# Performance work log

Hardware: AMD Instinct MI355X
Metric: run time of the kernel (lower is better)

The kernel has to match this reference:

```python
import jax, jax.numpy as jnp
import numpy as np

OBS_DIM = 4096
NUM_ACTIONS = 18
ACTION_DIM = 64
D_MODEL = 512
N_LAYERS = 4
HIST = 256
BATCH = 32
D_STATE = 16
D_CONV = 4
EXPAND = 2
D_INNER = EXPAND * D_MODEL           # 1024
DT_RANK = -(-D_MODEL // 16)          # ceil(512/16)=32
OBS_OUT = D_MODEL - ACTION_DIM       # 448


def setup_inputs() -> dict:
    key = jax.random.key(0)
    ks = jax.random.split(key, 16)
    s = 0.02
    inp = {
        "obss": jax.random.normal(ks[0], (BATCH, HIST, OBS_DIM), jnp.float32),
        "actions": jax.random.randint(ks[1], (BATCH, HIST, 1), 0, NUM_ACTIONS),
        "obs_W": jax.random.normal(ks[2], (OBS_OUT, OBS_DIM), jnp.float32) * s,
        "obs_b": jnp.zeros((OBS_OUT,), jnp.float32),
        "act_emb": jax.random.normal(ks[3], (NUM_ACTIONS, ACTION_DIM), jnp.float32) * s,
        "pos_emb": jax.random.normal(ks[4], (1, HIST, D_MODEL), jnp.float32) * s,
        # stacked Mamba params, leading dim = N_LAYERS
        "W_in": jax.random.normal(ks[5], (N_LAYERS, 2 * D_INNER, D_MODEL), jnp.float32) * s,
        "conv_w": jax.random.normal(ks[6], (N_LAYERS, D_INNER, D_CONV), jnp.float32) * s,
        "conv_b": jnp.zeros((N_LAYERS, D_INNER), jnp.float32),
        "W_x": jax.random.normal(ks[7], (N_LAYERS, DT_RANK + 2 * D_STATE, D_INNER), jnp.float32) * s,
        "W_dt": jax.random.normal(ks[8], (N_LAYERS, D_INNER, DT_RANK), jnp.float32) * s,
        "b_dt": jnp.full((N_LAYERS, D_INNER), -4.6, jnp.float32),  # softplus(-4.6)~0.01
        "A_log": jnp.log(jnp.broadcast_to(jnp.arange(1, D_STATE + 1, dtype=jnp.float32), (N_LAYERS, D_INNER, D_STATE))),
        "D_p": jnp.ones((N_LAYERS, D_INNER), jnp.float32),
        "W_out": jax.random.normal(ks[9], (N_LAYERS, D_MODEL, D_INNER), jnp.float32) * s,
        "ffn_W1": jax.random.normal(ks[10], (D_MODEL, D_MODEL), jnp.float32) * s,
        "ffn_b1": jnp.zeros((D_MODEL,), jnp.float32),
        "ffn_W2": jax.random.normal(ks[11], (NUM_ACTIONS, D_MODEL), jnp.float32) * s,
        "ffn_b2": jnp.zeros((NUM_ACTIONS,), jnp.float32),
    }
    return inp


def mamba_block(x, W_in, conv_w, conv_b, W_x, W_dt, b_dt, A_log, D_p, W_out):
    # x: (B, L, D_MODEL)
    B_, L, _ = x.shape
    xz = jnp.einsum('bld,ed->ble', x, W_in)            # (B,L,2*Di)
    xi, z = jnp.split(xz, 2, axis=-1)
    # causal depthwise conv1d, kernel D_CONV
    xp = jnp.pad(xi, ((0, 0), (D_CONV - 1, 0), (0, 0)))
    xc = conv_b + sum(conv_w[:, k] * xp[:, k:k + L, :] for k in range(D_CONV))
    xc = jax.nn.silu(xc)                               # (B,L,Di)
    xdbl = jnp.einsum('bld,ed->ble', xc, W_x)          # (B,L,dt_rank+2*ds)
    dt, Bm, Cm = jnp.split(xdbl, [DT_RANK, DT_RANK + D_STATE], axis=-1)
    dt = jax.nn.softplus(jnp.einsum('blr,dr->bld', dt, W_dt) + b_dt)  # (B,L,Di)
    A = -jnp.exp(A_log)                                # (Di,ds)

    def step(h, inp):
        dt_t, B_t, C_t, x_t = inp                      # (B,Di),(B,ds),(B,ds),(B,Di)
        dA = jnp.exp(dt_t[:, :, None] * A)             # (B,Di,ds)
        h = dA * h + dt_t[:, :, None] * B_t[:, None, :] * x_t[:, :, None]
        y = jnp.einsum('bdn,bn->bd', h, C_t)
        return h, y

    h0 = jnp.zeros((B_, D_INNER, D_STATE), xc.dtype)
    xs = (dt.transpose(1, 0, 2), Bm.transpose(1, 0, 2),
          Cm.transpose(1, 0, 2), xc.transpose(1, 0, 2))
    _, ys = jax.lax.scan(step, h0, xs)                 # (L,B,Di)
    y = ys.transpose(1, 0, 2) + xc * D_p
    y = y * jax.nn.silu(z)
    return jnp.einsum('bld,ed->ble', y, W_out)         # (B,L,D_MODEL)


def reference(obss, actions, obs_W, obs_b, act_emb, pos_emb, W_in, conv_w, conv_b,
              W_x, W_dt, b_dt, A_log, D_p, W_out, ffn_W1, ffn_b1, ffn_W2, ffn_b2):
    L = obss.shape[1]
    tok = jnp.einsum('blo,eo->ble', obss, obs_W) + obs_b          # (B,L,448)
    ae = act_emb[actions[:, :, 0]]                                # (B,L,64)
    # torch.roll(ae, 1, 1) with first step zeroed (history_len > 1)
    ae = jnp.concatenate([jnp.zeros_like(ae[:, :1]), ae[:, :-1]], axis=1)
    x = jnp.concatenate([ae, tok], axis=-1) + pos_emb[:, :L, :]   # (B,L,512)
    for i in range(N_LAYERS):
        x = mamba_block(x, W_in[i], conv_w[i], conv_b[i], W_x[i], W_dt[i],
                        b_dt[i], A_log[i], D_p[i], W_out[i])
    h = jax.nn.relu(jnp.einsum('bld,ed->ble', x, ffn_W1) + ffn_b1)
    out = jnp.einsum('bld,ed->ble', h, ffn_W2) + ffn_b2           # (B,L,18)
    return out[:, -L:, :]
```

## Files before the change

### kernel.cpp

```cpp
#include <hip/hip_runtime.h>
#include <hip/hip_bf16.h>
#include <cstdint>
#include <cstddef>

#define HIST    256
#define DMODEL  512
#define DINNER  1024
#define DSTATE  16
#define DTRANK  32
#define OBSDIM  4096
#define OBSOUT  448
#define ADIM    64
#define NLAYERS 4
#define MROWS   8192

typedef __bf16  bf16x8 __attribute__((ext_vector_type(8)));
typedef float   f32x4  __attribute__((ext_vector_type(4)));

enum { MEPI_TOK = 0, MEPI_BF16 = 1, MEPI_SPLIT = 2, MEPI_RELUB = 3, MEPI_PART = 4 };

__device__ __forceinline__ float siluf(float x) { return x / (1.f + __expf(-x)); }
__device__ __forceinline__ float softplusf(float x) {
    return fmaxf(x, 0.f) + log1pf(__expf(-fabsf(x)));
}
__device__ __forceinline__ float bflo(unsigned u) { return __uint_as_float(u << 16); }
__device__ __forceinline__ float bfhi(unsigned u) { return __uint_as_float(u & 0xffff0000u); }

template<int EPI, int NW>
__global__ __launch_bounds__(256)
void gemm_mfma(const __hip_bfloat16* __restrict__ A, int lda,
               const __hip_bfloat16* __restrict__ W,
               float* __restrict__ Cf, int ldc,
               __hip_bfloat16* __restrict__ Cb, int ldcb,
               int coff, int N, int K, int nbn,
               const float* __restrict__ bias, const float* __restrict__ pos)
{
    constexpr int MI = (NW == 128) ? 4 : 2;
    __shared__ __hip_bfloat16 Asm[2][128 * 32];
    __shared__ __hip_bfloat16 Bsm[2][NW * 32];
    const int bid = blockIdx.x;
    const int xcd = bid & 7;
    const int s   = bid >> 3;
    int n_blk, m_blk, kc_ = 0;
    if constexpr (EPI == MEPI_PART) {
        m_blk = xcd * 8 + (s >> 2);
        kc_   = s & 3;
        n_blk = 0;
    } else {
        n_blk = s % nbn;
        m_blk = xcd * ((int)(gridDim.x >> 3) / nbn) + s / nbn;
    }
    const int m0 = m_blk * 128;
    const int n0 = n_blk * NW;

    const int tid  = threadIdx.x;
    const int lane = tid & 63;
    const int wv   = tid >> 6;
    const int wm   = (NW == 128) ? ((wv >> 1) << 6) : (wv << 5);
    const int wn   = (NW == 128) ? ((wv & 1) << 6) : 0;
    const int sr   = lane >> 2;
    const int scs  = (((lane & 3) ^ ((lane >> 4) & 3)) << 3);
    const int quad = lane >> 4;
    const int c16  = lane & 15;

    f32x4 acc[MI][4] = {};
    const __hip_bfloat16* aptr = A + (size_t)(m0 + wv * 16 + sr) * lda + scs + kc_ * 256;
    const __hip_bfloat16* bptr = W + (size_t)(n0 + wv * 16 + sr) * K + scs;

#define STAGE(K0, BUF) { \
    __hip_bfloat16* asml = Asm[BUF] + wv * 16 * 32; \
    __hip_bfloat16* bsml = Bsm[BUF] + wv * 16 * 32; \
    __builtin_amdgcn_global_load_lds( \
        (const __attribute__((address_space(1))) void*)(aptr + (K0)), \
        (__attribute__((address_space(3))) void*)(asml), 16, 0, 0); \
    __builtin_amdgcn_global_load_lds( \
        (const __attribute__((address_space(1))) void*)(aptr + (size_t)64 * lda + (K0)), \
        (__attribute__((address_space(3))) void*)(asml + 64 * 32), 16, 0, 0); \
    __builtin_amdgcn_global_load_lds( \
        (const __attribute__((address_space(1))) void*)(bptr + (K0)), \
        (__attribute__((address_space(3))) void*)(bsml), 16, 0, 0); \
    if (NW == 128) \
        __builtin_amdgcn_global_load_lds( \
            (const __attribute__((address_space(1))) void*)(bptr + (size_t)64 * K + (K0)), \
            (__attribute__((address_space(3))) void*)(bsml + 64 * 32), 16, 0, 0); \
    }

    STAGE(0, 0)
    int cur = 0;
    for (int k0 = 0; k0 < K; k0 += 32) {
        if (k0 + 32 < K) {
            STAGE(k0 + 32, cur ^ 1)
            if constexpr (NW == 128) asm volatile("s_waitcnt vmcnt(4)" ::: "memory");
            else                     asm volatile("s_waitcnt vmcnt(3)" ::: "memory");
        } else {
            asm volatile("s_waitcnt vmcnt(0)" ::: "memory");
        }
        __builtin_amdgcn_s_barrier();
        __builtin_amdgcn_sched_barrier(0);

        bf16x8 af[MI], bfr[4];
        #pragma unroll
        for (int i = 0; i < MI; ++i) {
            const int csw = ((quad ^ ((c16 >> 2) & 3)) << 3);
            af[i]  = *(const bf16x8*)(Asm[cur] + (wm + i * 16 + c16) * 32 + csw);
        }
        #pragma unroll
        for (int j = 0; j < 4; ++j) {
            const int csw = ((quad ^ ((c16 >> 2) & 3)) << 3);
            bfr[j] = *(const bf16x8*)(Bsm[cur] + (wn + j * 16 + c16) * 32 + csw);
        }
        #pragma unroll
        for (int i = 0; i < MI; ++i)
            #pragma unroll
            for (int j = 0; j < 4; ++j)
                acc[i][j] = __builtin_amdgcn_mfma_f32_16x16x32_bf16(af[i], bfr[j], acc[i][j], 0, 0, 0);

        __builtin_amdgcn_sched_barrier(0);
        __builtin_amdgcn_s_barrier();
        cur ^= 1;
    }
#undef STAGE

    #pragma unroll
    for (int i = 0; i < MI; ++i) {
        const int mbase = m0 + wm + i * 16 + quad * 4;
        #pragma unroll
        for (int j = 0; j < 4; ++j) {
            const int n = n0 + wn + j * 16 + c16;
            if (n < N) {
                #pragma unroll
                for (int r = 0; r < 4; ++r) {
                    const size_t m = mbase + r;
                    float v = acc[i][j][r];
                    if (EPI == MEPI_TOK) {
                        v += bias[n] + pos[(m & (HIST - 1)) * DMODEL + coff + n];
                        Cb[m * ldcb + coff + n] = __float2bfloat16(v);
                    } else if (EPI == MEPI_BF16) {
                        Cb[m * ldcb + n] = __float2bfloat16(v);
                    } else if (EPI == MEPI_SPLIT) {
                        if (n < DTRANK) Cf[m * 32 + n] = v;
                        else Cb[(m >> 1) * 64 + (n & 15) * 4 + (m & 1) * 2 + ((n >> 4) & 1)]
                                 = __float2bfloat16(v);
                    } else if (EPI == MEPI_PART) {
                        Cf[((size_t)kc_ * MROWS + m) * 64 + n] = v;
                    } else {
                        Cb[m * ldcb + n] = __float2bfloat16(fmaxf(v + bias[n], 0.f));
                    }
                }
            }
        }
    }
}

__global__ __launch_bounds__(256)
void combine_split_kernel(const float* __restrict__ p, float* __restrict__ xdt,
                          __hip_bfloat16* __restrict__ bcb)
{
    const int idx = blockIdx.x * 256 + threadIdx.x;
    const int m  = idx >> 4;
    const int n4 = (idx & 15) << 2;
    const float4 a = *(const float4*)(p + (size_t)m * 64 + n4);
    const float4 b = *(const float4*)(p + ((size_t)MROWS + m) * 64 + n4);
    const float4 c = *(const float4*)(p + ((size_t)2 * MROWS + m) * 64 + n4);
    const float4 d = *(const float4*)(p + ((size_t)3 * MROWS + m) * 64 + n4);
    const float v[4] = { a.x + b.x + c.x + d.x, a.y + b.y + c.y + d.y,
                         a.z + b.z + c.z + d.z, a.w + b.w + c.w + d.w };
    if (n4 < 32) {
        *(float4*)(xdt + (size_t)m * 32 + n4) = make_float4(v[0], v[1], v[2], v[3]);
    } else {
        #pragma unroll
        for (int j = 0; j < 4; ++j) {
            const int n = n4 + j;
            bcb[(m >> 1) * 64 + (n & 15) * 4 + (m & 1) * 2 + ((n >> 4) & 1)]
                = __float2bfloat16(v[j]);
        }
    }
}

__global__ __launch_bounds__(256)
void gemm_f32_sp(const float* __restrict__ A, int lda,
                 const float* __restrict__ W,
                 __hip_bfloat16* __restrict__ C, int ldc,
                 int N, int K, const float* __restrict__ bias)
{
    __shared__ float As[32][68];
    __shared__ float Ws[32][68];
    const int tid = threadIdx.x;
    const int tx = tid & 15, ty = tid >> 4;
    const int m0 = blockIdx.y * 64;
    const int n0 = blockIdx.x * 64;
    const int lr = tid >> 3;
    const int lc = (tid & 7) << 2;
    float acc[4][4] = {};
    for (int k0 = 0; k0 < K; k0 += 32) {
        const float4 a0 = *(const float4*)(A + (size_t)(m0 + lr) * lda + k0 + lc);
        const float4 a1 = *(const float4*)(A + (size_t)(m0 + lr + 32) * lda + k0 + lc);
        const float4 b0 = *(const float4*)(W + (size_t)(n0 + lr) * K + k0 + lc);
        const float4 b1 = *(const float4*)(W + (size_t)(n0 + lr + 32) * K + k0 + lc);
        __syncthreads();
        As[lc+0][lr] = a0.x; As[lc+1][lr] = a0.y; As[lc+2][lr] = a0.z; As[lc+3][lr] = a0.w;
        As[lc+0][lr+32] = a1.x; As[lc+1][lr+32] = a1.y; As[lc+2][lr+32] = a1.z; As[lc+3][lr+32] = a1.w;
        Ws[lc+0][lr] = b0.x; Ws[lc+1][lr] = b0.y; Ws[lc+2][lr] = b0.z; Ws[lc+3][lr] = b0.w;
        Ws[lc+0][lr+32] = b1.x; Ws[lc+1][lr+32] = b1.y; Ws[lc+2][lr+32] = b1.z; Ws[lc+3][lr+32] = b1.w;
        __syncthreads();
        #pragma unroll
        for (int k = 0; k < 32; ++k) {
            const float4 a4 = *(const float4*)&As[k][ty << 2];
            const float4 b4 = *(const float4*)&Ws[k][tx << 2];
            const float a[4] = {a4.x, a4.y, a4.z, a4.w};
            const float b[4] = {b4.x, b4.y, b4.z, b4.w};
            #pragma unroll
            for (int i = 0; i < 4; ++i)
                #pragma unroll
                for (int j = 0; j < 4; ++j)
                    acc[i][j] = fmaf(a[i], b[j], acc[i][j]);
        }
    }
    const int mb = m0 + (ty << 2);
    const int nb = n0 + (tx << 2);
    #pragma unroll
    for (int i = 0; i < 4; ++i) {
        const size_t m = mb + i;
        #pragma unroll
        for (int j = 0; j < 4; ++j) {
            const int n = nb + j;
            C[m * ldc + n] = __float2bfloat16(softplusf(acc[i][j] + bias[n]));
        }
    }
}

__global__ __launch_bounds__(256)
void cast_bf16_kernel(const float* __restrict__ src, __hip_bfloat16* __restrict__ dst, int n4)
{
    const int i = blockIdx.x * 256 + threadIdx.x;
    if (i >= n4) return;
    const float4 v = ((const float4*)src)[i];
    union { __hip_bfloat16 h[4]; short4 s; } o;
    o.h[0] = __float2bfloat16(v.x); o.h[1] = __float2bfloat16(v.y);
    o.h[2] = __float2bfloat16(v.z); o.h[3] = __float2bfloat16(v.w);
    ((short4*)dst)[i] = o.s;
}

__global__ __launch_bounds__(256)
void cast_pad_kernel(const float* __restrict__ src, __hip_bfloat16* __restrict__ dst,
                     int nrows, int K4, int total4)
{
    const int i = blockIdx.x * 256 + threadIdx.x;
    if (i >= total4) return;
    const int row = i / K4;
    float4 v = make_float4(0.f, 0.f, 0.f, 0.f);
    if (row < nrows) v = ((const float4*)src)[i];
    union { __hip_bfloat16 h[4]; short4 s; } o;
    o.h[0] = __float2bfloat16(v.x); o.h[1] = __float2bfloat16(v.y);
    o.h[2] = __float2bfloat16(v.z); o.h[3] = __float2bfloat16(v.w);
    ((short4*)dst)[i] = o.s;
}

__global__ __launch_bounds__(256)
void embed_kernel(const int* __restrict__ actions, const float* __restrict__ act_emb,
                  const float* __restrict__ pos_emb, __hip_bfloat16* __restrict__ xb)
{
    const int idx = blockIdx.x * 256 + threadIdx.x;
    const int e = idx & 63;
    const int m = idx >> 6;
    const int l = m & (HIST - 1);
    const int b = m >> 8;
    float v = pos_emb[l * DMODEL + e];
    if (l > 0) {
        const int a = actions[b * HIST + l - 1];
        v += act_emb[a * ADIM + e];
    }
    xb[(size_t)m * DMODEL + e] = __float2bfloat16(v);
}

__global__ __launch_bounds__(256)
void conv_silu_kernel(const __hip_bfloat16* __restrict__ xzb, const float* __restrict__ cw,
                      const float* __restrict__ cb, __hip_bfloat16* __restrict__ xcb)
{
    const int idx = blockIdx.x * 256 + threadIdx.x;
    const int d = idx & (DINNER - 1);
    const int m = idx >> 10;
    const int l = m & (HIST - 1);
    const float4 w = ((const float4*)cw)[d];
    const __hip_bfloat16* basep = xzb + (size_t)m * (2 * DINNER) + d;
    float acc = cb[d] + w.w * __bfloat162float(basep[0]);
    if (l >= 1) acc = fmaf(w.z, __bfloat162float(basep[-2 * DINNER]), acc);
    if (l >= 2) acc = fmaf(w.y, __bfloat162float(basep[-4 * DINNER]), acc);
    if (l >= 3) acc = fmaf(w.x, __bfloat162float(basep[-6 * DINNER]), acc);
    xcb[idx] = __float2bfloat16(siluf(acc));
}

#define DPPA(x, CTRL) { float _t; \
    asm("v_add_f32_dpp %0, %1, %1 " CTRL " row_mask:0xf bank_mask:0xf" \
        : "=v"(_t) : "v"(x)); x = _t; }

__global__ __launch_bounds__(256)
void scan_kernel(const __hip_bfloat16* __restrict__ dtb, const __hip_bfloat16* __restrict__ bcb,
                 const __hip_bfloat16* __restrict__ xcb, const __hip_bfloat16* __restrict__ zb,
                 const float* __restrict__ A_log, const float* __restrict__ D_p,
                 __hip_bfloat16* __restrict__ yb)
{
    __shared__ unsigned sdx[2][16][68];
    __shared__ unsigned sbc[2][16][68];

    const int tid = threadIdx.x;
    const int n   = tid & 15;
    const int g   = tid >> 4;

    const int bid = blockIdx.x;
    const int blk = ((bid & 7) << 8) | (bid >> 3);
    const int c0  = blk * 16;
    const int b   = c0 >> 10;
    const int d0  = c0 & (DINNER - 1);
    const int d   = d0 + g;
    const size_t row0 = (size_t)b * HIST;

    const int sr = tid >> 2;
    const int sq = tid & 3;
    const unsigned short* dtu = (const unsigned short*)dtb;
    const unsigned short* xcu = (const unsigned short*)xcb;
    const unsigned short* zu  = (const unsigned short*)zb;
    const unsigned*       bcu = (const unsigned*)bcb;

    const float Ar = -__expf(A_log[d * DSTATE + n]);
#if __has_builtin(__builtin_amdgcn_exp2f)
    const float A2 = Ar * 1.44269504089f;
#define DAEXP(x) __builtin_amdgcn_exp2f((x) * A2)
#else
#define DAEXP(x) __expf((x) * Ar)
#endif
    const float Dp = D_p[d];
    float h = 0.f;

    uint2 dv, xv; uint4 bv;
    unsigned short za[4], znx[4];

#define SLOAD(cc) { \
    const size_t rb = (row0 + (size_t)(cc) * 64 + sr) * DINNER + d0 + sq * 4; \
    dv = *(const uint2*)(dtu + rb); \
    xv = *(const uint2*)(xcu + rb); \
    bv = *(const uint4*)(bcu + row0 * 16 + (size_t)(cc) * 1024 + tid * 4); \
}
#define SWRITE(bb) { \
    const int ch = sq * 4; \
    sdx[bb][ch + 0][sr] = (dv.x & 0xffffu) | (xv.x << 16); \
    sdx[bb][ch + 1][sr] = (dv.x >> 16)     | (xv.x & 0xffff0000u); \
    sdx[bb][ch + 2][sr] = (dv.y & 0xffffu) | (xv.y << 16); \
    sdx[bb][ch + 3][sr] = (dv.y >> 16)     | (xv.y & 0xffff0000u); \
    const int e2 = (tid & 7) * 2, p2 = (tid >> 3) * 2; \
    sbc[bb][e2 + 0][p2 + 0] = bv.x; \
    sbc[bb][e2 + 0][p2 + 1] = bv.y; \
    sbc[bb][e2 + 1][p2 + 0] = bv.z; \
    sbc[bb][e2 + 1][p2 + 1] = bv.w; \
}
#define ZLOAD(cc, arr) { \
    _Pragma("unroll") \
    for (int w = 0; w < 4; ++w) \
        arr[w] = zu[(row0 + (size_t)(cc) * 64 + w * 16 + n) * (2 * DINNER) + d0 + g]; \
}
#define SSTEP(Q, R, KK) { \
    const float dt = bflo(Q), xc = bfhi(Q); \
    const float Bv = bflo(R), Cv = bfhi(R); \
    const float dA = DAEXP(dt); \
    h = fmaf(dA, h, dt * xc * Bv); \
    float ctr = h * Cv; \
    DPPA(ctr, "quad_perm:[1,0,3,2]") \
    DPPA(ctr, "quad_perm:[2,3,0,1]") \
    DPPA(ctr, "row_half_mirror") \
    DPPA(ctr, "row_mirror") \
    if (n == (KK)) yreg = ctr; \
}

    SLOAD(0)
    ZLOAD(0, za)
    SWRITE(0)
    __syncthreads();

    for (int c = 0; c < 4; ++c) {
        const int buf = c & 1;
        if (c < 3) { SLOAD(c + 1) ZLOAD(c + 1, znx) }

        const unsigned (*sdxc)[68] = sdx[buf];
        const unsigned (*sbcc)[68] = sbc[buf];
        #pragma unroll
        for (int w = 0; w < 4; ++w) {
            float yreg = 0.f;
            #pragma unroll
            for (int jq = 0; jq < 4; ++jq) {
                const uint4 qv = *(const uint4*)&sdxc[g][w * 16 + jq * 4];
                const uint4 rv = *(const uint4*)&sbcc[n][w * 16 + jq * 4];
                SSTEP(qv.x, rv.x, jq * 4 + 0)
                SSTEP(qv.y, rv.y, jq * 4 + 1)
                SSTEP(qv.z, rv.z, jq * 4 + 2)
                SSTEP(qv.w, rv.w, jq * 4 + 3)
            }
            const float xcf = bfhi(sdxc[g][w * 16 + n]);
            const float ze  = __uint_as_float((unsigned)za[w] << 16);
            yb[(row0 + c * 64 + w * 16 + n) * DINNER + d] =
                __float2bfloat16((yreg + xcf * Dp) * siluf(ze));
        }

        if (c < 3) SWRITE((c + 1) & 1)
        __syncthreads();
        #pragma unroll
        for (int w = 0; w < 4; ++w) za[w] = znx[w];
    }
#undef SLOAD
#undef SWRITE
#undef ZLOAD
#undef SSTEP
#undef DAEXP
}

__global__ __launch_bounds__(256)
void ffn2_kernel(const __hip_bfloat16* __restrict__ h, const float* __restrict__ W2,
                 const float* __restrict__ b2, float* __restrict__ out)
{
    const int idx = blockIdx.x * 256 + threadIdx.x;
    const int n = idx & 31;
    const int m = idx >> 5;
    if (n >= 18) return;
    const unsigned short* hr = (const unsigned short*)(h + (size_t)m * DMODEL);
    const float* wr = W2 + (size_t)n * DMODEL;
    float acc = b2[n];
    for (int k = 0; k < DMODEL; k += 8) {
        const uint4 hv = *(const uint4*)(hr + k);
        const float4 w0 = *(const float4*)(wr + k);
        const float4 w1 = *(const float4*)(wr + k + 4);
        acc = fmaf(bflo(hv.x), w0.x, acc);
        acc = fmaf(bfhi(hv.x), w0.y, acc);
        acc = fmaf(bflo(hv.y), w0.z, acc);
        acc = fmaf(bfhi(hv.y), w0.w, acc);
        acc = fmaf(bflo(hv.z), w1.x, acc);
        acc = fmaf(bfhi(hv.z), w1.y, acc);
        acc = fmaf(bflo(hv.w), w1.z, acc);
        acc = fmaf(bfhi(hv.w), w1.w, acc);
    }
    out[(size_t)m * 18 + n] = acc;
}

extern "C" void kernel_launch(void* const* d_in, const int* in_sizes, int n_in,
                              void* d_out, int out_size, void* d_ws, size_t ws_size,
                              hipStream_t stream)
{
    const float* obss    = (const float*)d_in[0];
    const int*   actions = (const int*)  d_in[1];
    const float* obs_W   = (const float*)d_in[2];
    const float* obs_b   = (const float*)d_in[3];
    const float* act_emb = (const float*)d_in[4];
    const float* pos_emb = (const float*)d_in[5];
    const float* W_in    = (const float*)d_in[6];
    const float* conv_w  = (const float*)d_in[7];
    const float* conv_b  = (const float*)d_in[8];
    const float* W_x     = (const float*)d_in[9];
    const float* W_dt    = (const float*)d_in[10];
    const float* b_dt    = (const float*)d_in[11];
    const float* A_log   = (const float*)d_in[12];
    const float* D_p     = (const float*)d_in[13];
    const float* W_out   = (const float*)d_in[14];
    const float* ffn_W1  = (const float*)d_in[15];
    const float* ffn_b1  = (const float*)d_in[16];
    const float* ffn_W2  = (const float*)d_in[17];
    const float* ffn_b2  = (const float*)d_in[18];
    float* out = (float*)d_out;

    const size_t MiB = 1024 * 1024;
    char* base = (char*)d_ws;
    __hip_bfloat16* xb    = (__hip_bfloat16*)(base);
    __hip_bfloat16* xzb   = (__hip_bfloat16*)(base + 8 * MiB);
    __hip_bfloat16* xcb   = (__hip_bfloat16*)(base + 40 * MiB);
    __hip_bfloat16* dtb   = (__hip_bfloat16*)(base + 56 * MiB);
    __hip_bfloat16* yb    = (__hip_bfloat16*)(base + 88 * MiB);
    float*          xdt   = (float*)(base + 104 * MiB);
    __hip_bfloat16* bcb   = (__hip_bfloat16*)(base + 105 * MiB);
    __hip_bfloat16* wbuf  = (__hip_bfloat16*)(base + 106 * MiB);
    __hip_bfloat16* wxb   = (__hip_bfloat16*)(base + 110 * MiB);
    float*          xdtp  = (float*)(base + 112 * MiB);
    __hip_bfloat16* obssb = (__hip_bfloat16*)(base + 8 * MiB);
    __hip_bfloat16* hbuf  = (__hip_bfloat16*)(base + 8 * MiB);

    cast_bf16_kernel<<<(MROWS * OBSDIM / 4) / 256, 256, 0, stream>>>(obss, obssb, MROWS * OBSDIM / 4);
    cast_pad_kernel<<<(512 * OBSDIM / 4) / 256, 256, 0, stream>>>(obs_W, wbuf, OBSOUT, OBSDIM / 4, 512 * OBSDIM / 4);
    embed_kernel<<<MROWS * ADIM / 256, 256, 0, stream>>>(actions, act_emb, pos_emb, xb);
    gemm_mfma<MEPI_TOK, 64><<<8 * (MROWS / 128), 256, 0, stream>>>(
        obssb, OBSDIM, wbuf, nullptr, 0, xb, DMODEL, ADIM, OBSOUT, OBSDIM, 8, obs_b, pos_emb);

    for (int i = 0; i < NLAYERS; ++i) {
        cast_bf16_kernel<<<(2 * DINNER * DMODEL / 4) / 256, 256, 0, stream>>>(
            W_in + (size_t)i * 2 * DINNER * DMODEL, wbuf, 2 * DINNER * DMODEL / 4);
        gemm_mfma<MEPI_BF16, 128><<<(2 * DINNER / 128) * (MROWS / 128), 256, 0, stream>>>(
            xb, DMODEL, wbuf, nullptr, 0, xzb, 2 * DINNER, 0, 2 * DINNER, DMODEL,
            2 * DINNER / 128, nullptr, nullptr);
        conv_silu_kernel<<<MROWS * DINNER / 256, 256, 0, stream>>>(
            xzb, conv_w + (size_t)i * DINNER * 4, conv_b + (size_t)i * DINNER, xcb);
        cast_pad_kernel<<<(128 * DINNER / 4) / 256, 256, 0, stream>>>(
            W_x + (size_t)i * 64 * DINNER, wxb, 64, DINNER / 4, 128 * DINNER / 4);
        gemm_mfma<MEPI_PART, 64><<<256, 256, 0, stream>>>(
            xcb, DINNER, wxb, xdtp, 0, nullptr, 0, 0, 64, 256, 1, nullptr, nullptr);
        combine_split_kernel<<<MROWS * 16 / 256, 256, 0, stream>>>(xdtp, xdt, bcb);
        gemm_f32_sp<<<dim3(DINNER / 64, MROWS / 64), 256, 0, stream>>>(
            xdt, 32, W_dt + (size_t)i * DINNER * DTRANK, dtb, DINNER, DINNER, DTRANK,
            b_dt + (size_t)i * DINNER);
        scan_kernel<<<(32 * DINNER) / 16, 256, 0, stream>>>(
            dtb, bcb, xcb, xzb + DINNER, A_log + (size_t)i * DINNER * DSTATE,
            D_p + (size_t)i * DINNER, yb);
        cast_bf16_kernel<<<(DMODEL * DINNER / 4) / 256, 256, 0, stream>>>(
            W_out + (size_t)i * DMODEL * DINNER, wbuf, DMODEL * DINNER / 4);
        gemm_mfma<MEPI_BF16, 64><<<(DMODEL / 64) * (MROWS / 128), 256, 0, stream>>>(
            yb, DINNER, wbuf, nullptr, 0, xb, DMODEL, 0, DMODEL, DINNER,
            DMODEL / 64, nullptr, nullptr);
    }

    cast_bf16_kernel<<<(DMODEL * DMODEL / 4) / 256, 256, 0, stream>>>(ffn_W1, wbuf, DMODEL * DMODEL / 4);
    gemm_mfma<MEPI_RELUB, 64><<<(DMODEL / 64) * (MROWS / 128), 256, 0, stream>>>(
        xb, DMODEL, wbuf, nullptr, 0, hbuf, DMODEL, 0, DMODEL, DMODEL,
        DMODEL / 64, ffn_b1, nullptr);
    ffn2_kernel<<<MROWS * 32 / 256, 256, 0, stream>>>(hbuf, ffn_W2, ffn_b2, out);
}
```

Baseline: 1.143 ms.

## Deepen GEMM global-to-LDS pipeline from double to quad buffering

The MFMA GEMM used to stage one K-tile ahead with two LDS buffers. It now keeps three tiles in flight across four LDS buffers, with vmcnt waits adjusted to match, and drains the last tiles in an explicit epilogue. The aim is to hide more global-memory latency behind MFMA work. In exchange, LDS use per block doubles, which may cut occupancy, and the epilogue assumes K is at least 96.

```diff
diff --git a/kernel.cpp b/kernel.cpp
--- a/kernel.cpp
+++ b/kernel.cpp
@@ -36,8 +36,8 @@
                const float* __restrict__ bias, const float* __restrict__ pos)
 {
     constexpr int MI = (NW == 128) ? 4 : 2;
-    __shared__ __hip_bfloat16 Asm[2][128 * 32];
-    __shared__ __hip_bfloat16 Bsm[2][NW * 32];
+    __shared__ __hip_bfloat16 Asm[4][128 * 32];
+    __shared__ __hip_bfloat16 Bsm[4][NW * 32];
     const int bid = blockIdx.x;
     const int xcd = bid & 7;
     const int s   = bid >> 3;
@@ -85,40 +85,43 @@
             (__attribute__((address_space(3))) void*)(bsml + 64 * 32), 16, 0, 0); \
     }
 
-    STAGE(0, 0)
-    int cur = 0;
-    for (int k0 = 0; k0 < K; k0 += 32) {
-        if (k0 + 32 < K) {
-            STAGE(k0 + 32, cur ^ 1)
-            if constexpr (NW == 128) asm volatile("s_waitcnt vmcnt(4)" ::: "memory");
-            else                     asm volatile("s_waitcnt vmcnt(3)" ::: "memory");
-        } else {
-            asm volatile("s_waitcnt vmcnt(0)" ::: "memory");
-        }
+    auto kstep = [&](int buf) {
         __builtin_amdgcn_s_barrier();
         __builtin_amdgcn_sched_barrier(0);
-
         bf16x8 af[MI], bfr[4];
-        #pragma unroll
-        for (int i = 0; i < MI; ++i) {
-            const int csw = ((quad ^ ((c16 >> 2) & 3)) << 3);
-            af[i]  = *(const bf16x8*)(Asm[cur] + (wm + i * 16 + c16) * 32 + csw);
-        }
-        #pragma unroll
-        for (int j = 0; j < 4; ++j) {
-            const int csw = ((quad ^ ((c16 >> 2) & 3)) << 3);
-            bfr[j] = *(const bf16x8*)(Bsm[cur] + (wn + j * 16 + c16) * 32 + csw);
-        }
+        const int csw = ((quad ^ ((c16 >> 2) & 3)) << 3);
+        #pragma unroll
+        for (int i = 0; i < MI; ++i)
+            af[i]  = *(const bf16x8*)(Asm[buf] + (wm + i * 16 + c16) * 32 + csw);
+        #pragma unroll
+        for (int j = 0; j < 4; ++j)
+            bfr[j] = *(const bf16x8*)(Bsm[buf] + (wn + j * 16 + c16) * 32 + csw);
         #pragma unroll
         for (int i = 0; i < MI; ++i)
             #pragma unroll
             for (int j = 0; j < 4; ++j)
                 acc[i][j] = __builtin_amdgcn_mfma_f32_16x16x32_bf16(af[i], bfr[j], acc[i][j], 0, 0, 0);
-
         __builtin_amdgcn_sched_barrier(0);
         __builtin_amdgcn_s_barrier();
-        cur ^= 1;
-    }
+    };
+
+    const int NT = K >> 5;
+    STAGE(0, 0) STAGE(32, 1) STAGE(64, 2)
+    int it = 0;
+    for (; it + 3 < NT; ++it) {
+        STAGE((it + 3) << 5, (it + 3) & 3)
+        if constexpr (NW == 128) asm volatile("s_waitcnt vmcnt(12)" ::: "memory");
+        else                     asm volatile("s_waitcnt vmcnt(9)"  ::: "memory");
+        kstep(it & 3);
+    }
+    if constexpr (NW == 128) asm volatile("s_waitcnt vmcnt(8)" ::: "memory");
+    else                     asm volatile("s_waitcnt vmcnt(6)" ::: "memory");
+    kstep(it & 3); ++it;
+    if constexpr (NW == 128) asm volatile("s_waitcnt vmcnt(4)" ::: "memory");
+    else                     asm volatile("s_waitcnt vmcnt(3)" ::: "memory");
+    kstep(it & 3); ++it;
+    asm volatile("s_waitcnt vmcnt(0)" ::: "memory");
+    kstep(it & 3);
 #undef STAGE
 
     #pragma unroll
```

Result: no change. 1.138 ms (-0.4%).
